# Performance work log

Hardware: AMD Instinct MI355X
Metric: run time of the kernel (lower is better)

## Reference

```python
import jax, jax.numpy as jnp
import numpy as np

B, H, T, K, V = 2, 8, 2048, 128, 128


def setup_inputs() -> dict:
    key = jax.random.key(0)
    k1, k2, k3, k4, k5 = jax.random.split(key, 5)
    return {
        "q": jax.random.normal(k1, (B, H, T, K), dtype=jnp.float32),
        "k": jax.random.normal(k2, (B, H, T, K), dtype=jnp.float32),
        "v": jax.random.normal(k3, (B, H, T, V), dtype=jnp.float32),
        "i_gate": jax.random.normal(k4, (B, H, T), dtype=jnp.float32),
        "f_gate": jax.random.normal(k5, (B, H, T), dtype=jnp.float32),
    }


def reference(q, k, v, i_gate, f_gate):
    # Stabilized parallel mLSTM (same math as the chunked Triton kernel,
    # expressed in natural-log base instead of base-2).
    Bq, Hq, Tq, Kd = q.shape
    scale = Kd ** -0.5
    logf = jax.nn.log_sigmoid(f_gate)                      # [B,H,T]
    fc = jnp.cumsum(logf, axis=-1)                         # cumulative forget logits
    # log decay matrix: logD[t,s] = i[s] + (fc[t] - fc[s]) for s <= t
    logD = fc[..., :, None] - fc[..., None, :] + i_gate[..., None, :]  # [B,H,T,T]
    mask = jnp.tril(jnp.ones((Tq, Tq), dtype=bool))
    logD_masked = jnp.where(mask, logD, -jnp.inf)
    m = jnp.max(logD_masked, axis=-1)                      # row-wise stabilizer [B,H,T]
    D = jnp.where(mask, jnp.exp(logD - m[..., None]), 0.0) # stabilized decay matrix
    S = jnp.einsum("bhtk,bhsk->bhts", q, k) * scale * D    # gated scores
    norm = jnp.maximum(jnp.abs(jnp.sum(S, axis=-1)), jnp.exp(-m))  # [B,H,T]
    h = jnp.einsum("bhts,bhsv->bhtv", S, v) / norm[..., None]
    return h
```

## Files before the change

kernel.cpp:

```cpp
#include <hip/hip_runtime.h>

#define T_SEQ 2048
#define DHEAD 128
#define NBH 16
#define SCALE 0.08838834764831845f

typedef unsigned short u16;
typedef unsigned int u32;
typedef u16 u16x4 __attribute__((ext_vector_type(4)));
typedef u16 u16x8 __attribute__((ext_vector_type(8)));
typedef u32 u32x2 __attribute__((ext_vector_type(2)));
typedef short s16x4 __attribute__((ext_vector_type(4)));
typedef __bf16 bf16x8 __attribute__((ext_vector_type(8)));
typedef float f32x4 __attribute__((ext_vector_type(4)));

__device__ __forceinline__ u16 f2bfu(float x) {
  union { float f; unsigned u; } c; c.f = x;
  unsigned u = c.u;
  u = u + 0x7FFFu + ((u >> 16) & 1u);
  return (u16)(u >> 16);
}

__device__ __forceinline__ u32 packbf2(float lo, float hi) {
  return (u32)f2bfu(lo) | ((u32)f2bfu(hi) << 16);
}

__device__ __forceinline__ bf16x8 ldsFrag(const u16* p) {
  u16x8 t = *(const u16x8*)p;
  return __builtin_bit_cast(bf16x8, t);
}

__device__ __forceinline__ f32x4 mfma16x16x16bf16(s16x4 a, s16x4 b, f32x4 c) {
#if __has_builtin(__builtin_amdgcn_mfma_f32_16x16x16bf16_1k)
  return __builtin_amdgcn_mfma_f32_16x16x16bf16_1k(a, b, c, 0, 0, 0);
#else
  asm("v_mfma_f32_16x16x16_bf16 %0, %1, %2, %0" : "+v"(c) : "v"(a), "v"(b));
  return c;
#endif
}

__device__ __forceinline__ void gld_lds16(const void* g, void* l) {
  __builtin_amdgcn_global_load_lds(
      (__attribute__((address_space(1))) const unsigned int*)g,
      (__attribute__((address_space(3))) unsigned int*)l, 16, 0, 0);
}

__global__ __launch_bounds__(256) void gate_scan_kernel(
    const float* __restrict__ ig, const float* __restrict__ fg,
    float* __restrict__ a_out, float* __restrict__ c_out,
    float* __restrict__ fc_out)
{
  const int bh  = blockIdx.x;
  const int tid = threadIdx.x;
  const int base = bh * T_SEQ + tid * 8;
  __shared__ float sbuf[256];

  float lf[8];
  float run = 0.f;
#pragma unroll
  for (int j = 0; j < 8; ++j) {
    float x  = fg[base + j];
    float ls = fminf(x, 0.f) - log1pf(expf(-fabsf(x)));
    run += ls; lf[j] = run;
  }
  sbuf[tid] = run; __syncthreads();
  for (int off = 1; off < 256; off <<= 1) {
    float t = (tid >= off) ? sbuf[tid - off] : 0.f;
    __syncthreads();
    sbuf[tid] += t;
    __syncthreads();
  }
  const float excl = (tid > 0) ? sbuf[tid - 1] : 0.f;
  __syncthreads();

  float fc[8], cm[8];
  float runm = -INFINITY;
#pragma unroll
  for (int j = 0; j < 8; ++j) {
    fc[j] = excl + lf[j];
    fc_out[base + j] = fc[j];
    float av = ig[base + j] - fc[j];
    a_out[base + j] = av;
    runm = fmaxf(runm, av);
    cm[j] = runm;
  }
  sbuf[tid] = runm; __syncthreads();
  for (int off = 1; off < 256; off <<= 1) {
    float t = (tid >= off) ? sbuf[tid - off] : -INFINITY;
    __syncthreads();
    sbuf[tid] = fmaxf(sbuf[tid], t);
    __syncthreads();
  }
  const float exclm = (tid > 0) ? sbuf[tid - 1] : -INFINITY;
#pragma unroll
  for (int j = 0; j < 8; ++j) {
    c_out[base + j] = fmaxf(exclm, cm[j]);
  }
}

__global__ __launch_bounds__(256) void cvt_k_kernel(
    const float* __restrict__ src, const float* __restrict__ ag,
    const float* __restrict__ cg, u16* __restrict__ dst)
{
  const int i = (blockIdx.x * 256 + threadIdx.x) * 4;
  const int bhs = i >> 7;
  const float sc = __expf(ag[bhs] - cg[bhs | 63]);
  const float4 x = *(const float4*)(src + i);
  u16x4 p;
  p[0] = f2bfu(x.x * sc); p[1] = f2bfu(x.y * sc);
  p[2] = f2bfu(x.z * sc); p[3] = f2bfu(x.w * sc);
  *(u16x4*)(dst + i) = p;
}

__global__ __launch_bounds__(256) void cvt_vt_kernel(
    const float* __restrict__ v, u16* __restrict__ vt)
{
  const int bh = blockIdx.y, kt = blockIdx.x, tid = threadIdx.x;
  __shared__ __align__(16) u16 L[128 * 72];
  const int n0 = (tid & 31) * 4, k0 = (tid >> 5) * 8;
  const float* vp = v + ((size_t)bh * T_SEQ + kt * 64 + k0) * DHEAD + n0;
  u16 tv[4][8];
#pragma unroll
  for (int rr = 0; rr < 8; ++rr) {
    const float4 x = *(const float4*)(vp + rr * DHEAD);
    tv[0][rr] = f2bfu(x.x); tv[1][rr] = f2bfu(x.y);
    tv[2][rr] = f2bfu(x.z); tv[3][rr] = f2bfu(x.w);
  }
#pragma unroll
  for (int j = 0; j < 4; ++j) {
    u16x8 p;
#pragma unroll
    for (int rr = 0; rr < 8; ++rr) p[rr] = tv[j][rr];
    *(u16x8*)(&L[(n0 + j) * 72 + k0]) = p;
  }
  __syncthreads();
  const int row = tid >> 1, s0 = (tid & 1) * 32;
  u16* op = vt + ((size_t)bh * DHEAD + row) * T_SEQ + kt * 64 + s0;
#pragma unroll
  for (int i = 0; i < 4; ++i)
    *(u16x8*)(op + i * 8) = *(const u16x8*)(&L[row * 72 + s0 + i * 8]);
}

template <bool FAST>
__global__ __launch_bounds__(512, 1) void mlstm_fwd_kernel(
    const float* __restrict__ qg, const float* __restrict__ kxg,
    const float* __restrict__ vg,
    const u16* __restrict__ kbf, const u16* __restrict__ vtbf,
    const float* __restrict__ ag, const float* __restrict__ cg,
    const float* __restrict__ fcg, float* __restrict__ out)
{
  const int bx = (int)blockIdx.x;
  const int bh = bx & 15, p = bx >> 4;
  const int tid = (int)threadIdx.x;
  const int w8 = tid >> 6, lane = tid & 63;
  const int quad = lane >> 4, l16 = lane & 15;

  const int qsel = w8 >> 2;
  const int kg4  = w8 & 3;
  const int qt   = qsel ? p : (31 - p);
  const int nST  = 32 - p;
  const int qrow0 = qt * 64;

  __shared__ __align__(16) unsigned char SM[68096];

  const size_t hoff = (size_t)bh * T_SEQ * DHEAD;
  const int goff = bh * T_SEQ;

  bf16x8 qf[16];
#pragma unroll
  for (int nt = 0; nt < 4; ++nt) {
    const float* qp = qg + hoff + (size_t)(qrow0 + nt * 16 + l16) * DHEAD + quad * 8;
#pragma unroll
    for (int kc = 0; kc < 4; ++kc) {
      const float4 x0 = *(const float4*)(qp + kc * 32);
      const float4 x1 = *(const float4*)(qp + kc * 32 + 4);
      u16x8 t;
      t[0] = f2bfu(x0.x); t[1] = f2bfu(x0.y); t[2] = f2bfu(x0.z); t[3] = f2bfu(x0.w);
      t[4] = f2bfu(x1.x); t[5] = f2bfu(x1.y); t[6] = f2bfu(x1.z); t[7] = f2bfu(x1.w);
      qf[nt * 4 + kc] = __builtin_bit_cast(bf16x8, t);
    }
  }
  const float cmax = cg[goff + qt * 64 + 63];

  f32x4 oa[8][4];
#pragma unroll
  for (int mt = 0; mt < 8; ++mt)
#pragma unroll
    for (int nt = 0; nt < 4; ++nt) oa[mt][nt] = (f32x4){0.f, 0.f, 0.f, 0.f};
  float rsacc[4] = {0.f, 0.f, 0.f, 0.f};

  auto stage = [&](int st) {
    const int b = st & 1;
    u16* KbL = (u16*)(SM + b * 16384);
    u16* VbL = (u16*)(SM + 32768 + b * 16384);
    if (FAST) {
      const u16* ks = kbf + ((size_t)goff + st * 64) * DHEAD;
      const u16* vs = vtbf + (size_t)bh * DHEAD * T_SEQ + st * 64;
#pragma unroll
      for (int j = 0; j < 2; ++j) {
        const int B = (w8 * 2 + j) * 64 + lane;
        { const int key = B >> 4; const int db = (B & 15) ^ (key & 7);
          gld_lds16(ks + (size_t)key * DHEAD + db * 8, KbL + (w8 * 2 + j) * 512); }
        { const int n = B >> 3; const int kb = (B & 7) ^ (n & 7);
          gld_lds16(vs + (size_t)n * T_SEQ + kb * 8, VbL + (w8 * 2 + j) * 512); }
      }
    } else {
      const float ct = cg[goff + st * 64 + 63];
      const float* kp = kxg + hoff + (size_t)(st * 64) * DHEAD;
      const float* vp = vg + hoff + (size_t)(st * 64) * DHEAD;
#pragma unroll
      for (int j = 0; j < 2; ++j) {
        const int B = (w8 * 2 + j) * 64 + lane;
        { const int key = B >> 4; const int db = (B & 15) ^ (key & 7);
          const float sc = __expf(ag[goff + st * 64 + key] - ct);
          const float4 x0 = *(const float4*)(kp + (size_t)key * DHEAD + db * 8);
          const float4 x1 = *(const float4*)(kp + (size_t)key * DHEAD + db * 8 + 4);
          u16x8 pk;
          pk[0] = f2bfu(x0.x * sc); pk[1] = f2bfu(x0.y * sc);
          pk[2] = f2bfu(x0.z * sc); pk[3] = f2bfu(x0.w * sc);
          pk[4] = f2bfu(x1.x * sc); pk[5] = f2bfu(x1.y * sc);
          pk[6] = f2bfu(x1.z * sc); pk[7] = f2bfu(x1.w * sc);
          *(u16x8*)(KbL + B * 8) = pk; }
        { const int n = B >> 3; const int kb = (B & 7) ^ (n & 7);
          u16x8 pw;
#pragma unroll
          for (int rr = 0; rr < 8; ++rr)
            pw[rr] = f2bfu(vp[(size_t)(kb * 8 + rr) * DHEAD + n]);
          *(u16x8*)(VbL + B * 8) = pw; }
      }
    }
  };

  stage(0);
  __syncthreads();

  const int keyA = kg4 * 16 + l16;
  const int ksw  = l16 & 7;
  const int kbu  = kg4 * 2 + (quad >> 1);
  const int kofs = (quad & 1) * 4;

  for (int st = 0; st < nST; ++st) {
    const int b = st & 1;
    if (st + 1 < nST) stage(st + 1);

    if (st <= qt) {
      const u16* KbL = (const u16*)(SM + b * 16384);
      const u16* VbL = (const u16*)(SM + 32768 + b * 16384);

      f32x4 sa[4];
#pragma unroll
      for (int nt = 0; nt < 4; ++nt) sa[nt] = (f32x4){0.f, 0.f, 0.f, 0.f};
#pragma unroll
      for (int kc = 0; kc < 4; ++kc) {
        const bf16x8 kf = ldsFrag(KbL + keyA * 128 + (((kc * 4 + quad) ^ ksw) * 8));
        sa[0] = __builtin_amdgcn_mfma_f32_16x16x32_bf16(kf, qf[0 * 4 + kc], sa[0], 0, 0, 0);
        sa[1] = __builtin_amdgcn_mfma_f32_16x16x32_bf16(kf, qf[1 * 4 + kc], sa[1], 0, 0, 0);
        sa[2] = __builtin_amdgcn_mfma_f32_16x16x32_bf16(kf, qf[2 * 4 + kc], sa[2], 0, 0, 0);
        sa[3] = __builtin_amdgcn_mfma_f32_16x16x32_bf16(kf, qf[3 * 4 + kc], sa[3], 0, 0, 0);
      }

      const float etile = SCALE * __expf(cg[goff + st * 64 + 63] - cmax);
      const bool diag = (st == qt);

      s16x4 pfr[4];
#pragma unroll
      for (int nt = 0; nt < 4; ++nt) {
        float x0 = sa[nt][0] * etile, x1 = sa[nt][1] * etile;
        float x2 = sa[nt][2] * etile, x3 = sa[nt][3] * etile;
        if (diag) {
          const int qr = nt * 16 + l16, kb0 = kg4 * 16 + quad * 4;
          if (kb0 + 0 > qr) x0 = 0.f;
          if (kb0 + 1 > qr) x1 = 0.f;
          if (kb0 + 2 > qr) x2 = 0.f;
          if (kb0 + 3 > qr) x3 = 0.f;
        }
        rsacc[nt] += (x0 + x1) + (x2 + x3);
        pfr[nt] = __builtin_bit_cast(s16x4, (u32x2){packbf2(x0, x1), packbf2(x2, x3)});
      }

#pragma unroll
      for (int mt = 0; mt < 8; ++mt) {
        const int vd = mt * 16 + l16;
        const s16x4 va = *(const s16x4*)(VbL + vd * 64 + ((kbu ^ (vd & 7)) * 8) + kofs);
        oa[mt][0] = mfma16x16x16bf16(va, pfr[0], oa[mt][0]);
        oa[mt][1] = mfma16x16x16bf16(va, pfr[1], oa[mt][1]);
        oa[mt][2] = mfma16x16x16bf16(va, pfr[2], oa[mt][2]);
        oa[mt][3] = mfma16x16x16bf16(va, pfr[3], oa[mt][3]);
      }
    }
    __syncthreads();
  }

  float rst[4];
#pragma unroll
  for (int nt = 0; nt < 4; ++nt) {
    float x = rsacc[nt];
    x += __shfl_xor(x, 16, 64);
    x += __shfl_xor(x, 32, 64);
    rst[nt] = x;
  }
  float* rshp = (float*)(SM + 66048);
  if (lane < 16) {
#pragma unroll
    for (int nt = 0; nt < 4; ++nt)
      rshp[qsel * 256 + kg4 * 64 + nt * 16 + lane] = rst[nt];
  }
  __syncthreads();

  float inv[4] = {0.f, 0.f, 0.f, 0.f};
  if (kg4 == 3) {
#pragma unroll
    for (int nt = 0; nt < 4; ++nt) {
      const int row = nt * 16 + l16;
      const float tot = rshp[qsel * 256 + row] + rshp[qsel * 256 + 64 + row]
                      + rshp[qsel * 256 + 128 + row] + rshp[qsel * 256 + 192 + row];
      const float nf = __expf(-(cmax + fcg[goff + qrow0 + row]));
      inv[nt] = 1.f / fmaxf(fabsf(tot), nf);
    }
  }

  float* osh = (float*)SM;
  const int obase = qsel * 64 * 129;
  for (int r = 0; r < 4; ++r) {
    if (kg4 == r) {
#pragma unroll
      for (int mt = 0; mt < 8; ++mt)
#pragma unroll
        for (int nt = 0; nt < 4; ++nt)
#pragma unroll
          for (int rg = 0; rg < 4; ++rg) {
            const int row = nt * 16 + l16;
            const int vd = mt * 16 + quad * 4 + rg;
            const int ad = obase + row * 129 + vd;
            float v = oa[mt][nt][rg];
            if (r > 0) v += osh[ad];
            if (r == 3) v *= inv[nt];
            osh[ad] = v;
          }
    }
    __syncthreads();
  }

  {
    const int col = tid & 31;
    const int rg0 = tid >> 5;
#pragma unroll
    for (int i = 0; i < 8; ++i) {
      const int ra = rg0 + 16 * i;
      const int tile = ra >> 6, row = ra & 63;
      const int qtt = tile ? p : (31 - p);
      const float* lp = osh + (tile * 64 + row) * 129 + col * 4;
      float4 v; v.x = lp[0]; v.y = lp[1]; v.z = lp[2]; v.w = lp[3];
      *(float4*)(out + hoff + (size_t)(qtt * 64 + row) * DHEAD + col * 4) = v;
    }
  }
}

extern "C" void kernel_launch(void* const* d_in, const int* in_sizes, int n_in,
                              void* d_out, int out_size, void* d_ws, size_t ws_size,
                              hipStream_t stream) {
  const float* q  = (const float*)d_in[0];
  const float* k  = (const float*)d_in[1];
  const float* v  = (const float*)d_in[2];
  const float* ig = (const float*)d_in[3];
  const float* fg = (const float*)d_in[4];

  const size_t gate_bytes = (size_t)3 * NBH * T_SEQ * sizeof(float);
  const size_t kv_elems   = (size_t)NBH * T_SEQ * DHEAD;
  const bool fast = ws_size >= gate_bytes + 2 * kv_elems * sizeof(u16);

  float* a_ws  = (float*)d_ws;
  float* c_ws  = a_ws + NBH * T_SEQ;
  float* fc_ws = c_ws + NBH * T_SEQ;
  u16* kbf  = (u16*)((char*)d_ws + gate_bytes);
  u16* vtbf = kbf + kv_elems;

  gate_scan_kernel<<<dim3(NBH), dim3(256), 0, stream>>>(ig, fg, a_ws, c_ws, fc_ws);
  if (fast) {
    cvt_k_kernel<<<dim3((unsigned)(kv_elems / 1024)), dim3(256), 0, stream>>>(
        k, a_ws, c_ws, kbf);
    cvt_vt_kernel<<<dim3(T_SEQ / 64, NBH), dim3(256), 0, stream>>>(v, vtbf);
    mlstm_fwd_kernel<true><<<dim3(256), dim3(512), 0, stream>>>(
        q, k, v, kbf, vtbf, a_ws, c_ws, fc_ws, (float*)d_out);
  } else {
    mlstm_fwd_kernel<false><<<dim3(256), dim3(512), 0, stream>>>(
        q, k, v, kbf, vtbf, a_ws, c_ws, fc_ws, (float*)d_out);
  }
}
```

Before: 151.6 us.

## Process paired query tiles sequentially with 16 waves and warp-shuffle gate scan

The main kernel now runs 1024 threads per block. Each of 16 waves owns a 16-row query strip by 16-key slice, and the block handles the two paired query tiles one after the other in a single 33-step staged loop, instead of both tiles at once with 8 waves each holding 4 row tiles. This cuts per-wave accumulator registers and runs more waves per CU. The cost is a serialized second tile pass with its own epilogue and extra barriers. The gate scan kernel also moves from a shared-memory Hillis-Steele scan to wave shuffles with 1024 threads.

After: 147.1 us. 1.03x faster.

```diff
diff --git a/kernel.cpp b/kernel.cpp
--- a/kernel.cpp
+++ b/kernel.cpp
@@ -45,57 +45,58 @@
       (__attribute__((address_space(3))) unsigned int*)l, 16, 0, 0);
 }
 
-__global__ __launch_bounds__(256) void gate_scan_kernel(
+__global__ __launch_bounds__(1024) void gate_scan_kernel(
     const float* __restrict__ ig, const float* __restrict__ fg,
     float* __restrict__ a_out, float* __restrict__ c_out,
     float* __restrict__ fc_out)
 {
-  const int bh  = blockIdx.x;
-  const int tid = threadIdx.x;
-  const int base = bh * T_SEQ + tid * 8;
-  __shared__ float sbuf[256];
-
-  float lf[8];
-  float run = 0.f;
-#pragma unroll
-  for (int j = 0; j < 8; ++j) {
-    float x  = fg[base + j];
-    float ls = fminf(x, 0.f) - log1pf(expf(-fabsf(x)));
-    run += ls; lf[j] = run;
-  }
-  sbuf[tid] = run; __syncthreads();
-  for (int off = 1; off < 256; off <<= 1) {
-    float t = (tid >= off) ? sbuf[tid - off] : 0.f;
-    __syncthreads();
-    sbuf[tid] += t;
-    __syncthreads();
-  }
-  const float excl = (tid > 0) ? sbuf[tid - 1] : 0.f;
+  const int bh = blockIdx.x, tid = threadIdx.x;
+  const int w = tid >> 6, lane = tid & 63;
+  const int base = bh * T_SEQ + tid * 2;
+  __shared__ float wsum[16];
+  __shared__ float wmax[16];
+
+  const float x0 = fg[base], x1 = fg[base + 1];
+  const float ls0 = fminf(x0, 0.f) - log1pf(expf(-fabsf(x0)));
+  const float ls1 = fminf(x1, 0.f) - log1pf(expf(-fabsf(x1)));
+  const float s = ls0 + ls1;
+
+  float sc = s;
+#pragma unroll
+  for (int off = 1; off < 64; off <<= 1) {
+    const float t = __shfl_up(sc, off, 64);
+    if (lane >= off) sc += t;
+  }
+  if (lane == 63) wsum[w] = sc;
   __syncthreads();
-
-  float fc[8], cm[8];
-  float runm = -INFINITY;
-#pragma unroll
-  for (int j = 0; j < 8; ++j) {
-    fc[j] = excl + lf[j];
-    fc_out[base + j] = fc[j];
-    float av = ig[base + j] - fc[j];
-    a_out[base + j] = av;
-    runm = fmaxf(runm, av);
-    cm[j] = runm;
-  }
-  sbuf[tid] = runm; __syncthreads();
-  for (int off = 1; off < 256; off <<= 1) {
-    float t = (tid >= off) ? sbuf[tid - off] : -INFINITY;
-    __syncthreads();
-    sbuf[tid] = fmaxf(sbuf[tid], t);
-    __syncthreads();
-  }
-  const float exclm = (tid > 0) ? sbuf[tid - 1] : -INFINITY;
-#pragma unroll
-  for (int j = 0; j < 8; ++j) {
-    c_out[base + j] = fmaxf(exclm, cm[j]);
-  }
+  float wo = 0.f;
+#pragma unroll
+  for (int i = 0; i < 15; ++i) if (i < w) wo += wsum[i];
+  const float excl = wo + (sc - s);
+  const float fc0 = excl + ls0;
+  const float fc1 = excl + ls0 + ls1;
+  fc_out[base] = fc0; fc_out[base + 1] = fc1;
+  const float a0 = ig[base] - fc0;
+  const float a1 = ig[base + 1] - fc1;
+  a_out[base] = a0; a_out[base + 1] = a1;
+
+  const float m = fmaxf(a0, a1);
+  float mc = m;
+#pragma unroll
+  for (int off = 1; off < 64; off <<= 1) {
+    const float t = __shfl_up(mc, off, 64);
+    if (lane >= off) mc = fmaxf(mc, t);
+  }
+  if (lane == 63) wmax[w] = mc;
+  __syncthreads();
+  float wmo = -INFINITY;
+#pragma unroll
+  for (int i = 0; i < 15; ++i) if (i < w) wmo = fmaxf(wmo, wmax[i]);
+  const float prev = __shfl_up(mc, 1, 64);
+  float exclm = (lane > 0) ? prev : -INFINITY;
+  exclm = fmaxf(exclm, wmo);
+  c_out[base] = fmaxf(exclm, a0);
+  c_out[base + 1] = fmaxf(exclm, m);
 }
 
 __global__ __launch_bounds__(256) void cvt_k_kernel(
@@ -142,7 +143,7 @@
 }
 
 template <bool FAST>
-__global__ __launch_bounds__(512, 1) void mlstm_fwd_kernel(
+__global__ __launch_bounds__(1024, 4) void mlstm_fwd_kernel(
     const float* __restrict__ qg, const float* __restrict__ kxg,
     const float* __restrict__ vg,
     const u16* __restrict__ kbf, const u16* __restrict__ vtbf,
@@ -152,24 +153,25 @@
   const int bx = (int)blockIdx.x;
   const int bh = bx & 15, p = bx >> 4;
   const int tid = (int)threadIdx.x;
-  const int w8 = tid >> 6, lane = tid & 63;
+  const int w = tid >> 6, lane = tid & 63;
   const int quad = lane >> 4, l16 = lane & 15;
-
-  const int qsel = w8 >> 2;
-  const int kg4  = w8 & 3;
-  const int qt   = qsel ? p : (31 - p);
-  const int nST  = 32 - p;
-  const int qrow0 = qt * 64;
-
-  __shared__ __align__(16) unsigned char SM[68096];
+  const int kg = w & 3, rq = w >> 2;
+
+  const int qtA = 31 - p, qtB = p;
+  const int nA = qtA + 1;
+
+  __shared__ __align__(16) unsigned char SM[99584];
+  u16* Kst = (u16*)SM;
+  u16* Vst = (u16*)(SM + 32768);
+  float* osh = (float*)(SM + 65536);
+  float* rsh = (float*)(SM + 98560);
 
   const size_t hoff = (size_t)bh * T_SEQ * DHEAD;
   const int goff = bh * T_SEQ;
 
-  bf16x8 qf[16];
-#pragma unroll
-  for (int nt = 0; nt < 4; ++nt) {
-    const float* qp = qg + hoff + (size_t)(qrow0 + nt * 16 + l16) * DHEAD + quad * 8;
+  bf16x8 qf[4];
+  auto loadQ = [&](int lqt) {
+    const float* qp = qg + hoff + (size_t)(lqt * 64 + rq * 16 + l16) * DHEAD + quad * 8;
 #pragma unroll
     for (int kc = 0; kc < 4; ++kc) {
       const float4 x0 = *(const float4*)(qp + kc * 32);
@@ -177,183 +179,151 @@
       u16x8 t;
       t[0] = f2bfu(x0.x); t[1] = f2bfu(x0.y); t[2] = f2bfu(x0.z); t[3] = f2bfu(x0.w);
       t[4] = f2bfu(x1.x); t[5] = f2bfu(x1.y); t[6] = f2bfu(x1.z); t[7] = f2bfu(x1.w);
-      qf[nt * 4 + kc] = __builtin_bit_cast(bf16x8, t);
-    }
-  }
-  const float cmax = cg[goff + qt * 64 + 63];
-
-  f32x4 oa[8][4];
-#pragma unroll
-  for (int mt = 0; mt < 8; ++mt)
-#pragma unroll
-    for (int nt = 0; nt < 4; ++nt) oa[mt][nt] = (f32x4){0.f, 0.f, 0.f, 0.f};
-  float rsacc[4] = {0.f, 0.f, 0.f, 0.f};
-
-  auto stage = [&](int st) {
-    const int b = st & 1;
-    u16* KbL = (u16*)(SM + b * 16384);
-    u16* VbL = (u16*)(SM + 32768 + b * 16384);
+      qf[kc] = __builtin_bit_cast(bf16x8, t);
+    }
+  };
+
+  f32x4 oa[8];
+  float rsacc;
+  auto zeroAcc = [&]() {
+#pragma unroll
+    for (int mt = 0; mt < 8; ++mt) oa[mt] = (f32x4){0.f, 0.f, 0.f, 0.f};
+    rsacc = 0.f;
+  };
+  zeroAcc();
+
+  auto stage = [&](int st, int b) {
+    u16* KbL = Kst + b * 8192;
+    u16* VbL = Vst + b * 8192;
     if (FAST) {
       const u16* ks = kbf + ((size_t)goff + st * 64) * DHEAD;
       const u16* vs = vtbf + (size_t)bh * DHEAD * T_SEQ + st * 64;
-#pragma unroll
-      for (int j = 0; j < 2; ++j) {
-        const int B = (w8 * 2 + j) * 64 + lane;
-        { const int key = B >> 4; const int db = (B & 15) ^ (key & 7);
-          gld_lds16(ks + (size_t)key * DHEAD + db * 8, KbL + (w8 * 2 + j) * 512); }
-        { const int n = B >> 3; const int kb = (B & 7) ^ (n & 7);
-          gld_lds16(vs + (size_t)n * T_SEQ + kb * 8, VbL + (w8 * 2 + j) * 512); }
-      }
+      { const int key = tid >> 4; const int db = (tid & 15) ^ (key & 7);
+        gld_lds16(ks + (size_t)key * DHEAD + db * 8, KbL + w * 512); }
+      { const int n = tid >> 3; const int kb = (tid & 7) ^ (n & 7);
+        gld_lds16(vs + (size_t)n * T_SEQ + kb * 8, VbL + w * 512); }
     } else {
       const float ct = cg[goff + st * 64 + 63];
       const float* kp = kxg + hoff + (size_t)(st * 64) * DHEAD;
       const float* vp = vg + hoff + (size_t)(st * 64) * DHEAD;
-#pragma unroll
-      for (int j = 0; j < 2; ++j) {
-        const int B = (w8 * 2 + j) * 64 + lane;
-        { const int key = B >> 4; const int db = (B & 15) ^ (key & 7);
-          const float sc = __expf(ag[goff + st * 64 + key] - ct);
-          const float4 x0 = *(const float4*)(kp + (size_t)key * DHEAD + db * 8);
-          const float4 x1 = *(const float4*)(kp + (size_t)key * DHEAD + db * 8 + 4);
-          u16x8 pk;
-          pk[0] = f2bfu(x0.x * sc); pk[1] = f2bfu(x0.y * sc);
-          pk[2] = f2bfu(x0.z * sc); pk[3] = f2bfu(x0.w * sc);
-          pk[4] = f2bfu(x1.x * sc); pk[5] = f2bfu(x1.y * sc);
-          pk[6] = f2bfu(x1.z * sc); pk[7] = f2bfu(x1.w * sc);
-          *(u16x8*)(KbL + B * 8) = pk; }
-        { const int n = B >> 3; const int kb = (B & 7) ^ (n & 7);
-          u16x8 pw;
-#pragma unroll
-          for (int rr = 0; rr < 8; ++rr)
-            pw[rr] = f2bfu(vp[(size_t)(kb * 8 + rr) * DHEAD + n]);
-          *(u16x8*)(VbL + B * 8) = pw; }
-      }
-    }
-  };
-
-  stage(0);
-  __syncthreads();
-
-  const int keyA = kg4 * 16 + l16;
+      { const int key = tid >> 4; const int db = (tid & 15) ^ (key & 7);
+        const float sc = __expf(ag[goff + st * 64 + key] - ct);
+        const float4 x0 = *(const float4*)(kp + (size_t)key * DHEAD + db * 8);
+        const float4 x1 = *(const float4*)(kp + (size_t)key * DHEAD + db * 8 + 4);
+        u16x8 pk;
+        pk[0] = f2bfu(x0.x * sc); pk[1] = f2bfu(x0.y * sc);
+        pk[2] = f2bfu(x0.z * sc); pk[3] = f2bfu(x0.w * sc);
+        pk[4] = f2bfu(x1.x * sc); pk[5] = f2bfu(x1.y * sc);
+        pk[6] = f2bfu(x1.z * sc); pk[7] = f2bfu(x1.w * sc);
+        *(u16x8*)(KbL + tid * 8) = pk; }
+      { const int n = tid >> 3; const int kb = (tid & 7) ^ (n & 7);
+        u16x8 pw;
+#pragma unroll
+        for (int rr = 0; rr < 8; ++rr)
+          pw[rr] = f2bfu(vp[(size_t)(kb * 8 + rr) * DHEAD + n]);
+        *(u16x8*)(VbL + tid * 8) = pw; }
+    }
+  };
+
+  const int keyA = kg * 16 + l16;
   const int ksw  = l16 & 7;
-  const int kbu  = kg4 * 2 + (quad >> 1);
+  const int kbu  = kg * 2 + (quad >> 1);
   const int kofs = (quad & 1) * 4;
 
-  for (int st = 0; st < nST; ++st) {
-    const int b = st & 1;
-    if (st + 1 < nST) stage(st + 1);
-
-    if (st <= qt) {
-      const u16* KbL = (const u16*)(SM + b * 16384);
-      const u16* VbL = (const u16*)(SM + 32768 + b * 16384);
-
-      f32x4 sa[4];
-#pragma unroll
-      for (int nt = 0; nt < 4; ++nt) sa[nt] = (f32x4){0.f, 0.f, 0.f, 0.f};
-#pragma unroll
-      for (int kc = 0; kc < 4; ++kc) {
-        const bf16x8 kf = ldsFrag(KbL + keyA * 128 + (((kc * 4 + quad) ^ ksw) * 8));
-        sa[0] = __builtin_amdgcn_mfma_f32_16x16x32_bf16(kf, qf[0 * 4 + kc], sa[0], 0, 0, 0);
-        sa[1] = __builtin_amdgcn_mfma_f32_16x16x32_bf16(kf, qf[1 * 4 + kc], sa[1], 0, 0, 0);
-        sa[2] = __builtin_amdgcn_mfma_f32_16x16x32_bf16(kf, qf[2 * 4 + kc], sa[2], 0, 0, 0);
-        sa[3] = __builtin_amdgcn_mfma_f32_16x16x32_bf16(kf, qf[3 * 4 + kc], sa[3], 0, 0, 0);
-      }
-
-      const float etile = SCALE * __expf(cg[goff + st * 64 + 63] - cmax);
-      const bool diag = (st == qt);
-
-      s16x4 pfr[4];
-#pragma unroll
-      for (int nt = 0; nt < 4; ++nt) {
-        float x0 = sa[nt][0] * etile, x1 = sa[nt][1] * etile;
-        float x2 = sa[nt][2] * etile, x3 = sa[nt][3] * etile;
-        if (diag) {
-          const int qr = nt * 16 + l16, kb0 = kg4 * 16 + quad * 4;
-          if (kb0 + 0 > qr) x0 = 0.f;
-          if (kb0 + 1 > qr) x1 = 0.f;
-          if (kb0 + 2 > qr) x2 = 0.f;
-          if (kb0 + 3 > qr) x3 = 0.f;
-        }
-        rsacc[nt] += (x0 + x1) + (x2 + x3);
-        pfr[nt] = __builtin_bit_cast(s16x4, (u32x2){packbf2(x0, x1), packbf2(x2, x3)});
-      }
-
-#pragma unroll
-      for (int mt = 0; mt < 8; ++mt) {
-        const int vd = mt * 16 + l16;
-        const s16x4 va = *(const s16x4*)(VbL + vd * 64 + ((kbu ^ (vd & 7)) * 8) + kofs);
-        oa[mt][0] = mfma16x16x16bf16(va, pfr[0], oa[mt][0]);
-        oa[mt][1] = mfma16x16x16bf16(va, pfr[1], oa[mt][1]);
-        oa[mt][2] = mfma16x16x16bf16(va, pfr[2], oa[mt][2]);
-        oa[mt][3] = mfma16x16x16bf16(va, pfr[3], oa[mt][3]);
-      }
-    }
-    __syncthreads();
-  }
-
-  float rst[4];
-#pragma unroll
-  for (int nt = 0; nt < 4; ++nt) {
-    float x = rsacc[nt];
+  auto computeTile = [&](int cqt, int st, int b, float ccmax) {
+    const u16* KbL = Kst + b * 8192;
+    const u16* VbL = Vst + b * 8192;
+
+    f32x4 sa = (f32x4){0.f, 0.f, 0.f, 0.f};
+#pragma unroll
+    for (int kc = 0; kc < 4; ++kc) {
+      const bf16x8 kf = ldsFrag(KbL + keyA * 128 + (((kc * 4 + quad) ^ ksw) * 8));
+      sa = __builtin_amdgcn_mfma_f32_16x16x32_bf16(kf, qf[kc], sa, 0, 0, 0);
+    }
+
+    const float etile = SCALE * __expf(cg[goff + st * 64 + 63] - ccmax);
+    float x0 = sa[0] * etile, x1 = sa[1] * etile;
+    float x2 = sa[2] * etile, x3 = sa[3] * etile;
+    if (st == cqt) {
+      const int qr = rq * 16 + l16, kb0 = kg * 16 + quad * 4;
+      if (kb0 + 0 > qr) x0 = 0.f;
+      if (kb0 + 1 > qr) x1 = 0.f;
+      if (kb0 + 2 > qr) x2 = 0.f;
+      if (kb0 + 3 > qr) x3 = 0.f;
+    }
+    rsacc += (x0 + x1) + (x2 + x3);
+    const s16x4 pfr = __builtin_bit_cast(s16x4, (u32x2){packbf2(x0, x1), packbf2(x2, x3)});
+
+#pragma unroll
+    for (int mt = 0; mt < 8; ++mt) {
+      const int vd = mt * 16 + l16;
+      const s16x4 va = *(const s16x4*)(VbL + vd * 64 + ((kbu ^ (vd & 7)) * 8) + kofs);
+      oa[mt] = mfma16x16x16bf16(va, pfr, oa[mt]);
+    }
+  };
+
+  auto epilogue = [&](int eqt, float ecmax) {
+    float x = rsacc;
     x += __shfl_xor(x, 16, 64);
     x += __shfl_xor(x, 32, 64);
-    rst[nt] = x;
-  }
-  float* rshp = (float*)(SM + 66048);
-  if (lane < 16) {
-#pragma unroll
-    for (int nt = 0; nt < 4; ++nt)
-      rshp[qsel * 256 + kg4 * 64 + nt * 16 + lane] = rst[nt];
-  }
-  __syncthreads();
-
-  float inv[4] = {0.f, 0.f, 0.f, 0.f};
-  if (kg4 == 3) {
-#pragma unroll
-    for (int nt = 0; nt < 4; ++nt) {
-      const int row = nt * 16 + l16;
-      const float tot = rshp[qsel * 256 + row] + rshp[qsel * 256 + 64 + row]
-                      + rshp[qsel * 256 + 128 + row] + rshp[qsel * 256 + 192 + row];
-      const float nf = __expf(-(cmax + fcg[goff + qrow0 + row]));
-      inv[nt] = 1.f / fmaxf(fabsf(tot), nf);
-    }
-  }
-
-  float* osh = (float*)SM;
-  const int obase = qsel * 64 * 129;
-  for (int r = 0; r < 4; ++r) {
-    if (kg4 == r) {
-#pragma unroll
-      for (int mt = 0; mt < 8; ++mt)
-#pragma unroll
-        for (int nt = 0; nt < 4; ++nt)
+    if (lane < 16) rsh[kg * 64 + rq * 16 + lane] = x;
+    __syncthreads();
+    float inv = 0.f;
+    if (kg == 3) {
+      const int row = rq * 16 + l16;
+      const float tot = rsh[row] + rsh[64 + row] + rsh[128 + row] + rsh[192 + row];
+      const float nf = __expf(-(ecmax + fcg[goff + eqt * 64 + row]));
+      inv = 1.f / fmaxf(fabsf(tot), nf);
+    }
+    for (int r = 0; r < 4; ++r) {
+      if (kg == r) {
+#pragma unroll
+        for (int mt = 0; mt < 8; ++mt)
 #pragma unroll
           for (int rg = 0; rg < 4; ++rg) {
-            const int row = nt * 16 + l16;
+            const int row = rq * 16 + l16;
             const int vd = mt * 16 + quad * 4 + rg;
-            const int ad = obase + row * 129 + vd;
-            float v = oa[mt][nt][rg];
+            const int ad = row * 129 + vd;
+            float v = oa[mt][rg];
             if (r > 0) v += osh[ad];
-            if (r == 3) v *= inv[nt];
+            if (r == 3) v *= inv;
             osh[ad] = v;
           }
-    }
+      }
+      __syncthreads();
+    }
+    const int col = tid & 31, r0 = tid >> 5;
+#pragma unroll
+    for (int i = 0; i < 2; ++i) {
+      const int row = r0 + 32 * i;
+      const float* lp = osh + row * 129 + col * 4;
+      float4 v; v.x = lp[0]; v.y = lp[1]; v.z = lp[2]; v.w = lp[3];
+      *(float4*)(out + hoff + (size_t)(eqt * 64 + row) * DHEAD + col * 4) = v;
+    }
+  };
+
+  int qt = qtA;
+  float cmax = cg[goff + qtA * 64 + 63];
+  loadQ(qtA);
+  stage(0, 0);
+  __syncthreads();
+
+  for (int it = 0; it < 33; ++it) {
+    if (it < 32) {
+      const int nx = it + 1;
+      stage((nx < nA) ? nx : nx - nA, nx & 1);
+    }
+    computeTile(qt, (it < nA) ? it : it - nA, it & 1, cmax);
     __syncthreads();
-  }
-
-  {
-    const int col = tid & 31;
-    const int rg0 = tid >> 5;
-#pragma unroll
-    for (int i = 0; i < 8; ++i) {
-      const int ra = rg0 + 16 * i;
-      const int tile = ra >> 6, row = ra & 63;
-      const int qtt = tile ? p : (31 - p);
-      const float* lp = osh + (tile * 64 + row) * 129 + col * 4;
-      float4 v; v.x = lp[0]; v.y = lp[1]; v.z = lp[2]; v.w = lp[3];
-      *(float4*)(out + hoff + (size_t)(qtt * 64 + row) * DHEAD + col * 4) = v;
-    }
-  }
+    if (it == nA - 1) {
+      epilogue(qtA, cmax);
+      zeroAcc();
+      qt = qtB;
+      cmax = cg[goff + qtB * 64 + 63];
+      loadQ(qtB);
+    }
+  }
+  epilogue(qtB, cmax);
 }
 
 extern "C" void kernel_launch(void* const* d_in, const int* in_sizes, int n_in,
@@ -375,15 +345,15 @@
   u16* kbf  = (u16*)((char*)d_ws + gate_bytes);
   u16* vtbf = kbf + kv_elems;
 
-  gate_scan_kernel<<<dim3(NBH), dim3(256), 0, stream>>>(ig, fg, a_ws, c_ws, fc_ws);
+  gate_scan_kernel<<<dim3(NBH), dim3(1024), 0, stream>>>(ig, fg, a_ws, c_ws, fc_ws);
   if (fast) {
     cvt_k_kernel<<<dim3((unsigned)(kv_elems / 1024)), dim3(256), 0, stream>>>(
         k, a_ws, c_ws, kbf);
     cvt_vt_kernel<<<dim3(T_SEQ / 64, NBH), dim3(256), 0, stream>>>(v, vtbf);
-    mlstm_fwd_kernel<true><<<dim3(256), dim3(512), 0, stream>>>(
+    mlstm_fwd_kernel<true><<<dim3(256), dim3(1024), 0, stream>>>(
         q, k, v, kbf, vtbf, a_ws, c_ws, fc_ws, (float*)d_out);
   } else {
-    mlstm_fwd_kernel<false><<<dim3(256), dim3(512), 0, stream>>>(
+    mlstm_fwd_kernel<false><<<dim3(256), dim3(1024), 0, stream>>>(
         q, k, v, kbf, vtbf, a_ws, c_ws, fc_ws, (float*)d_out);
   }
 }
```
